# Optimization experiments

Measured on AMD Instinct MI355X. Metric: run time of the kernel, lower is better.

Reference implementation:

```python
import jax, jax.numpy as jnp
import numpy as np

B, S, H = 2, 2048, 4096
NH, HD = 32, 128          # heads, head_dim = H // NH
ROPE_THETA = 10000.0
CLIP_QKV = 8.0
SCALE = HD ** -0.5


def setup_inputs() -> dict:
    key = jax.random.key(0)
    k1, k2, k3 = jax.random.split(key, 3)
    hidden_states = jax.random.normal(k1, (B, S, H), dtype=jnp.float32)
    positions = jnp.arange(S, dtype=jnp.int32)
    # 0.02 init scale keeps qkv magnitudes realistic so the +/-8 clamp rarely saturates
    w_qkv = jax.random.normal(k2, (3 * H, H), dtype=jnp.float32) * 0.02
    w_o = jax.random.normal(k3, (H, H), dtype=jnp.float32) * 0.02
    return {"hidden_states": hidden_states, "positions": positions,
            "w_qkv": w_qkv, "w_o": w_o}


def _rope(x, positions):
    # x: [B, S, NH, HD]; neox-style rotary over full head_dim
    half = HD // 2
    inv_freq = 1.0 / (ROPE_THETA ** (jnp.arange(0, half, dtype=jnp.float32) / half))
    ang = positions.astype(jnp.float32)[:, None] * inv_freq[None, :]  # [S, half]
    cos = jnp.cos(ang)[None, :, None, :]
    sin = jnp.sin(ang)[None, :, None, :]
    x1, x2 = x[..., :half], x[..., half:]
    return jnp.concatenate([x1 * cos - x2 * sin, x2 * cos + x1 * sin], axis=-1)


def reference(hidden_states, positions, w_qkv, w_o):
    # fused QKV projection (no bias) + clamp
    qkv = jnp.einsum('bsh,oh->bso', hidden_states, w_qkv)
    qkv = jnp.clip(qkv, -CLIP_QKV, CLIP_QKV)
    q, k, v = jnp.split(qkv, 3, axis=-1)            # each [B, S, H]
    q = q.reshape(B, S, NH, HD)
    k = k.reshape(B, S, NH, HD)
    v = v.reshape(B, S, NH, HD)
    q = _rope(q, positions)
    k = _rope(k, positions)
    # causal attention
    scores = jnp.einsum('bqhd,bkhd->bhqk', q, k) * SCALE
    causal = jnp.tril(jnp.ones((S, S), dtype=bool))
    scores = jnp.where(causal[None, None], scores, jnp.finfo(scores.dtype).min)
    probs = jax.nn.softmax(scores, axis=-1)
    attn = jnp.einsum('bhqk,bkhd->bqhd', probs, v).reshape(B, S, H)
    return jnp.einsum('bsh,oh->bso', attn, w_o)
```

## Files before the change

### kernel.cpp

```cpp
#include <hip/hip_runtime.h>
#include <hip/hip_bf16.h>

#define BATCH 2
#define SEQ 2048
#define HID 4096
#define NHEAD 32
#define HDIM 128
#define BH (BATCH*NHEAD)
#define MROWS (BATCH*SEQ)
#define ATT_SCALE 0.08838834764831845f

typedef __attribute__((ext_vector_type(8))) short bf16x8;
typedef __attribute__((ext_vector_type(4))) float f32x4;

__device__ __forceinline__ float bf2f(short x){
  union { float f; unsigned u; } v; v.u = ((unsigned)(unsigned short)x) << 16; return v.f;
}
__device__ __forceinline__ short f2bf(float f){
  union { float f; unsigned u; } v; v.f = f;
  unsigned r = v.u + 0x7fffu + ((v.u >> 16) & 1u);
  return (short)(r >> 16);
}
__device__ __forceinline__ void gload_lds16(const void* g, void* l){
  __builtin_amdgcn_global_load_lds(
    (const __attribute__((address_space(1))) void*)g,
    (__attribute__((address_space(3))) void*)l, 16, 0, 0);
}

__global__ void cvt3_bf16(const float* __restrict__ a, short* __restrict__ ao, int na4,
                          const float* __restrict__ b, short* __restrict__ bo, int nb4,
                          const float* __restrict__ cc, short* __restrict__ co, int nc4){
  int i = blockIdx.x*blockDim.x + threadIdx.x;
  int stride = gridDim.x*blockDim.x;
  int tot = na4 + nb4 + nc4;
  for (; i < tot; i += stride){
    const float* src; short* dst; int k = i;
    if (k < na4){ src=a; dst=ao; }
    else if (k < na4+nb4){ k -= na4; src=b; dst=bo; }
    else { k -= na4+nb4; src=cc; dst=co; }
    float4 v = ((const float4*)src)[k];
    short4 o;
    o.x = f2bf(v.x); o.y = f2bf(v.y); o.z = f2bf(v.z); o.w = f2bf(v.w);
    ((short4*)dst)[k] = o;
  }
}

__global__ void rope_table_k(const int* __restrict__ pos, float* __restrict__ tab){
  int idx = blockIdx.x*blockDim.x + threadIdx.x;
  if (idx >= SEQ*64) return;
  int s = idx >> 6, d = idx & 63;
  float p = (float)pos[s];
  float inv = exp2f(-(float)d * (13.287712379549449f/64.0f));
  float ang = p * inv;
  tab[2*idx]   = cosf(ang);
  tab[2*idx+1] = sinf(ang);
}

template<int W>
__device__ __forceinline__ void stage_half(const short* __restrict__ gsrc, int ldg,
                                           short* lds, int tid, int h){
  #pragma unroll
  for (int li=0; li<2; ++li){
    int e16 = li*512 + tid;
    int rs = e16 >> 3, ck = e16 & 7;
    int r = ((rs/W)*2 + h)*W + (rs%W);
    gload_lds16(gsrc + (size_t)r*ldg + ((ck ^ (r&7))<<3),
                lds + r*64 + ck*8);
  }
}

__device__ __forceinline__ void read_ahalf(const short* Asb, int wr, int c, int g,
                                           int Mh, bf16x8 (&afr)[4][2]){
  #pragma unroll
  for (int mi=0; mi<4; ++mi){
    int row = wr*128 + (Mh*4+mi)*16 + c;
    const char* bp = (const char*)Asb + row*128;
    #pragma unroll
    for (int kk=0; kk<2; ++kk)
      afr[mi][kk] = *(const bf16x8*)(bp + ((kk*64 + g*16) ^ ((row&7)<<4)));
  }
}
__device__ __forceinline__ void read_bhalf(const short* Bsb, int wc, int c, int g,
                                           int Nh, bf16x8 (&bfr)[2][2]){
  #pragma unroll
  for (int ni=0; ni<2; ++ni){
    int row = wc*64 + (Nh*2+ni)*16 + c;
    const char* bp = (const char*)Bsb + row*128;
    #pragma unroll
    for (int kk=0; kk<2; ++kk)
      bfr[ni][kk] = *(const bf16x8*)(bp + ((kk*64 + g*16) ^ ((row&7)<<4)));
  }
}
template<int MH, int NHH>
__device__ __forceinline__ void mma_q(bf16x8 (&afr)[4][2], bf16x8 (&bfr)[2][2],
                                      f32x4 (&acc)[8][4]){
  #pragma unroll
  for (int kk=0; kk<2; ++kk)
    #pragma unroll
    for (int mi=0; mi<4; ++mi)
      #pragma unroll
      for (int ni=0; ni<2; ++ni)
        acc[MH*4+mi][NHH*2+ni] = __builtin_amdgcn_mfma_f32_16x16x32_bf16(
            afr[mi][kk], bfr[ni][kk], acc[MH*4+mi][NHH*2+ni], 0,0,0);
}

#define BAR()  asm volatile("s_barrier" ::: "memory")
#define LGK0() asm volatile("s_waitcnt lgkmcnt(0)" ::: "memory")
#define VMC6() asm volatile("s_waitcnt vmcnt(6)" ::: "memory")
#define VMC8() asm volatile("s_waitcnt vmcnt(8)" ::: "memory")
#define VMC0() asm volatile("s_waitcnt vmcnt(0)" ::: "memory")
#define SP1()  __builtin_amdgcn_s_setprio(1)
#define SP0()  __builtin_amdgcn_s_setprio(0)

template<int MODE>
__global__ __launch_bounds__(512, 2) void gemm8r(
    const short* __restrict__ A, const short* __restrict__ Bw,
    short* __restrict__ Qb, short* __restrict__ Kb, short* __restrict__ Vb,
    float* __restrict__ Of){
  __shared__ __align__(16) short As[2][256*64];
  __shared__ __align__(16) short Bs[2][256*64];
  const int K = HID;
  int tid = threadIdx.x, lane = tid & 63, w = tid >> 6;
  int wr = w >> 2, wc = w & 3, g = lane >> 4, c = lane & 15;
  int gx = gridDim.x;
  int nwg = gx * gridDim.y;
  int bid = blockIdx.y*gx + blockIdx.x;
  int cpx = nwg >> 3;
  int swz = (bid & 7)*cpx + (bid >> 3);
  int m0 = (swz / gx) * 256, n0 = (swz % gx) * 256;

  const short* Abase = A  + (size_t)m0*K;
  const short* Bbase = Bw + (size_t)n0*K;
  auto stageA = [&](int buf, int kt, int h){
    stage_half<64>(Abase + kt*64, K, &As[buf][0], tid, h);
  };
  auto stageB = [&](int buf, int kt, int h){
    stage_half<32>(Bbase + kt*64, K, &Bs[buf][0], tid, h);
  };

  f32x4 acc[8][4];
  f32x4 zero = {0.f,0.f,0.f,0.f};
  #pragma unroll
  for (int i=0;i<8;++i)
    #pragma unroll
    for (int j=0;j<4;++j) acc[i][j] = zero;
  bf16x8 afr[4][2], bfr0[2][2], bfr1[2][2];

  stageB(0,0,0); stageB(0,0,1); stageA(0,0,0); stageA(0,0,1);
  stageB(1,1,0); stageB(1,1,1); stageA(1,1,0); stageA(1,1,1);
  VMC8();
  BAR();

  const int NITER = K/128;
  for (int i = 0; i < NITER-1; ++i){
    int t2 = 2*i+2, t3 = 2*i+3;
    read_ahalf(&As[0][0], wr,c,g, 0, afr);
    read_bhalf(&Bs[0][0], wc,c,g, 0, bfr0);
    BAR(); LGK0(); SP1(); mma_q<0,0>(afr,bfr0,acc); SP0(); BAR();
    read_bhalf(&Bs[0][0], wc,c,g, 1, bfr1);
    stageB(0, t2, 0);
    BAR(); LGK0(); SP1(); mma_q<0,1>(afr,bfr1,acc); SP0(); BAR();
    read_ahalf(&As[0][0], wr,c,g, 1, afr);
    stageB(0, t2, 1); stageA(0, t2, 0);
    BAR(); LGK0(); SP1(); mma_q<1,1>(afr,bfr1,acc); SP0(); BAR();
    BAR(); LGK0(); SP1(); mma_q<1,0>(afr,bfr0,acc); SP0(); VMC6(); BAR();
    read_ahalf(&As[1][0], wr,c,g, 0, afr);
    read_bhalf(&Bs[1][0], wc,c,g, 0, bfr0);
    stageA(0, t2, 1);
    BAR(); LGK0(); SP1(); mma_q<0,0>(afr,bfr0,acc); SP0(); BAR();
    read_bhalf(&Bs[1][0], wc,c,g, 1, bfr1);
    stageB(1, t3, 0);
    BAR(); LGK0(); SP1(); mma_q<0,1>(afr,bfr1,acc); SP0(); BAR();
    read_ahalf(&As[1][0], wr,c,g, 1, afr);
    stageB(1, t3, 1); stageA(1, t3, 0);
    BAR(); LGK0(); SP1(); mma_q<1,1>(afr,bfr1,acc); SP0(); BAR();
    stageA(1, t3, 1);
    BAR(); LGK0(); SP1(); mma_q<1,0>(afr,bfr0,acc); SP0(); VMC8(); BAR();
  }
  {
    read_ahalf(&As[0][0], wr,c,g, 0, afr);
    read_bhalf(&Bs[0][0], wc,c,g, 0, bfr0);
    BAR(); LGK0(); SP1(); mma_q<0,0>(afr,bfr0,acc); SP0(); BAR();
    read_bhalf(&Bs[0][0], wc,c,g, 1, bfr1);
    BAR(); LGK0(); SP1(); mma_q<0,1>(afr,bfr1,acc); SP0(); BAR();
    read_ahalf(&As[0][0], wr,c,g, 1, afr);
    BAR(); LGK0(); SP1(); mma_q<1,1>(afr,bfr1,acc); SP0(); BAR();
    BAR(); LGK0(); SP1(); mma_q<1,0>(afr,bfr0,acc); SP0(); VMC0(); BAR();
    read_ahalf(&As[1][0], wr,c,g, 0, afr);
    read_bhalf(&Bs[1][0], wc,c,g, 0, bfr0);
    BAR(); LGK0(); SP1(); mma_q<0,0>(afr,bfr0,acc); SP0(); BAR();
    read_bhalf(&Bs[1][0], wc,c,g, 1, bfr1);
    BAR(); LGK0(); SP1(); mma_q<0,1>(afr,bfr1,acc); SP0(); BAR();
    read_ahalf(&As[1][0], wr,c,g, 1, afr);
    BAR(); LGK0(); SP1(); mma_q<1,1>(afr,bfr1,acc); SP0(); BAR();
    BAR(); LGK0(); SP1(); mma_q<1,0>(afr,bfr0,acc); SP0(); BAR();
  }

  #pragma unroll
  for (int fa=0; fa<8; ++fa){
    #pragma unroll
    for (int fb=0; fb<4; ++fb){
      f32x4 v = acc[fa][fb];
      #pragma unroll
      for (int rr=0; rr<4; ++rr){
        int row = m0 + wr*128 + fa*16 + g*4 + rr;
        int col = n0 + wc*64  + fb*16 + c;
        float x = v[rr];
        if (MODE == 0){
          x = fminf(fmaxf(x, -8.0f), 8.0f);
          int sel = col >> 12, wi = col & 4095;
          int head = wi >> 7, d = wi & 127;
          int b = row >> 11, s = row & 2047;
          size_t off = ((size_t)(b*NHEAD + head)*SEQ + s)*HDIM + d;
          short* dst = (sel == 0) ? Qb : (sel == 1) ? Kb : Vb;
          dst[off] = f2bf(x);
        } else {
          Of[(size_t)row*HID + col] = x;
        }
      }
    }
  }
}

__global__ void rope_apply_k(short* __restrict__ Qb, short* __restrict__ Kb,
                             const float* __restrict__ tab){
  int idx = blockIdx.x*blockDim.x + threadIdx.x;
  if (idx >= BH*SEQ*8) return;
  int t = idx & 7;
  int s = (idx >> 3) & (SEQ-1);
  int bh = idx >> 14;
  size_t base = ((size_t)bh*SEQ + s)*HDIM + t*8;
  const float* tb = tab + 2*(s*64 + t*8);
  bf16x8 q1 = *(bf16x8*)(Qb+base), q2 = *(bf16x8*)(Qb+base+64);
  bf16x8 k1 = *(bf16x8*)(Kb+base), k2 = *(bf16x8*)(Kb+base+64);
  bf16x8 o1, o2, p1, p2;
  #pragma unroll
  for (int u=0;u<8;++u){
    float cs = tb[2*u], sn = tb[2*u+1];
    float a = bf2f(q1[u]), b = bf2f(q2[u]);
    o1[u] = f2bf(a*cs - b*sn); o2[u] = f2bf(b*cs + a*sn);
    a = bf2f(k1[u]); b = bf2f(k2[u]);
    p1[u] = f2bf(a*cs - b*sn); p2[u] = f2bf(b*cs + a*sn);
  }
  *(bf16x8*)(Qb+base)    = o1; *(bf16x8*)(Qb+base+64) = o2;
  *(bf16x8*)(Kb+base)    = p1; *(bf16x8*)(Kb+base+64) = p2;
}

__global__ void transpose_v_k(const short* __restrict__ V, short* __restrict__ Vt){
  __shared__ short t[32][33];
  int bh = blockIdx.z;
  int s0 = blockIdx.x*32, d0 = blockIdx.y*32;
  int tx = threadIdx.x & 31, ty = threadIdx.x >> 5;
  const short* src = V + ((size_t)bh*SEQ + s0)*HDIM + d0;
  #pragma unroll
  for (int i=ty;i<32;i+=8) t[i][tx] = src[(size_t)i*HDIM + tx];
  __syncthreads();
  short* dst = Vt + ((size_t)bh*HDIM + d0)*SEQ + s0;
  #pragma unroll
  for (int i=ty;i<32;i+=8) dst[(size_t)i*SEQ + tx] = t[tx][i];
}

__global__ __launch_bounds__(256) void flash_attn_k(
    const short* __restrict__ Qb, const short* __restrict__ Kb,
    const short* __restrict__ Vt, short* __restrict__ attn){
  __shared__ short Ks[2][64*128];
  __shared__ short Vs[2][128*64];
  __shared__ short Ps[4][16][72];
  int tid = threadIdx.x, lane = tid & 63, w = tid >> 6;
  int g = lane >> 4, c = lane & 15;
  int flat = blockIdx.y*gridDim.x + blockIdx.x;
  int xcd = flat & 7, idx = flat >> 3;
  int bh = xcd + 8*(idx >> 5);
  int qblk = 31 - (idx & 31);
  int q0 = qblk * 64;
  int qw = q0 + w*16;
  bf16x8 qf[4];
  #pragma unroll
  for (int ks=0;ks<4;++ks)
    qf[ks] = *(const bf16x8*)(Qb + ((size_t)bh*SEQ + qw + c)*HDIM + ks*32 + g*8);
  f32x4 o[8];
  f32x4 zero = {0.f,0.f,0.f,0.f};
  #pragma unroll
  for (int i=0;i<8;++i) o[i] = zero;
  float m_r[4] = {-1e30f,-1e30f,-1e30f,-1e30f};
  float l_r[4] = {0.f,0.f,0.f,0.f};

  auto stage = [&](int j, int b){
    int kv0 = j*64;
    #pragma unroll
    for (int i=0;i<4;++i){
      int e = i*256 + tid;
      int kr = e >> 4, kc = e & 15;
      gload_lds16(Kb + ((size_t)bh*SEQ + kv0 + kr)*HDIM + (size_t)((kc ^ (kr&7))*8),
                  &Ks[b][kr*128 + kc*8]);
      int vr = e >> 3, vc = e & 7;
      gload_lds16(Vt + ((size_t)bh*HDIM + vr)*SEQ + kv0 + (size_t)((vc ^ (vr&7))*8),
                  &Vs[b][vr*64 + vc*8]);
    }
  };

  stage(0, 0);
  __syncthreads();
  int buf = 0;
  for (int j=0;j<=qblk;++j){
    if (j < qblk) stage(j+1, buf^1);

    int kv0 = j*64;
    f32x4 sf[4];
    #pragma unroll
    for (int fj=0;fj<4;++fj) sf[fj] = zero;
    __builtin_amdgcn_s_setprio(1);
    #pragma unroll
    for (int ks=0;ks<4;++ks){
      #pragma unroll
      for (int fj=0;fj<4;++fj){
        int kvrow = fj*16 + c;
        bf16x8 kb = *(const bf16x8*)&Ks[buf][kvrow*128 + (((ks*4+g) ^ (c&7))*8)];
        sf[fj] = __builtin_amdgcn_mfma_f32_16x16x32_bf16(qf[ks], kb, sf[fj], 0,0,0);
      }
    }
    __builtin_amdgcn_s_setprio(0);
    bool diag = (j == qblk);
    float rmax[4];
    #pragma unroll
    for (int rr=0;rr<4;++rr){
      #pragma unroll
      for (int fj=0;fj<4;++fj){
        float v = sf[fj][rr] * ATT_SCALE;
        if (diag && (kv0 + fj*16 + c) > (qw + g*4 + rr)) v = -1e30f;
        sf[fj][rr] = v;
      }
      float t = fmaxf(fmaxf(sf[0][rr], sf[1][rr]), fmaxf(sf[2][rr], sf[3][rr]));
      t = fmaxf(t, __shfl_xor(t, 1));
      t = fmaxf(t, __shfl_xor(t, 2));
      t = fmaxf(t, __shfl_xor(t, 4));
      t = fmaxf(t, __shfl_xor(t, 8));
      rmax[rr] = t;
    }
    float alpha[4];
    #pragma unroll
    for (int rr=0;rr<4;++rr){
      float mnew = fmaxf(m_r[rr], rmax[rr]);
      alpha[rr] = __expf(m_r[rr] - mnew);
      m_r[rr] = mnew;
      float ps = 0.f;
      #pragma unroll
      for (int fj=0;fj<4;++fj){
        float p = __expf(sf[fj][rr] - mnew);
        sf[fj][rr] = p;
        ps += p;
      }
      ps += __shfl_xor(ps, 1);
      ps += __shfl_xor(ps, 2);
      ps += __shfl_xor(ps, 4);
      ps += __shfl_xor(ps, 8);
      l_r[rr] = l_r[rr]*alpha[rr] + ps;
    }
    #pragma unroll
    for (int ni=0;ni<8;++ni){
      f32x4 t = o[ni];
      t[0]*=alpha[0]; t[1]*=alpha[1]; t[2]*=alpha[2]; t[3]*=alpha[3];
      o[ni] = t;
    }
    #pragma unroll
    for (int fj=0;fj<4;++fj)
      #pragma unroll
      for (int rr=0;rr<4;++rr)
        Ps[w][g*4+rr][fj*16+c] = f2bf(sf[fj][rr]);
    __builtin_amdgcn_s_setprio(1);
    #pragma unroll
    for (int ks=0;ks<2;++ks){
      bf16x8 pa = *(const bf16x8*)&Ps[w][c][ks*32 + g*8];
      #pragma unroll
      for (int ni=0;ni<8;++ni){
        int d = ni*16 + c;
        bf16x8 vb = *(const bf16x8*)&Vs[buf][d*64 + (((ks*4+g) ^ (c&7))*8)];
        o[ni] = __builtin_amdgcn_mfma_f32_16x16x32_bf16(pa, vb, o[ni], 0,0,0);
      }
    }
    __builtin_amdgcn_s_setprio(0);
    __syncthreads();
    buf ^= 1;
  }
  int b = bh >> 5, h = bh & 31;
  #pragma unroll
  for (int rr=0;rr<4;++rr){
    float inv = 1.0f / l_r[rr];
    int s = qw + g*4 + rr;
    #pragma unroll
    for (int ni=0;ni<8;++ni){
      int d = ni*16 + c;
      attn[((size_t)(b*SEQ + s))*HID + h*HDIM + d] = f2bf(o[ni][rr] * inv);
    }
  }
}

extern "C" void kernel_launch(void* const* d_in, const int* in_sizes, int n_in,
                              void* d_out, int out_size, void* d_ws, size_t ws_size,
                              hipStream_t stream){
  const float* hs   = (const float*)d_in[0];
  const int*   pos  = (const int*)d_in[1];
  const float* wqkv = (const float*)d_in[2];
  const float* wo   = (const float*)d_in[3];
  float* out = (float*)d_out;
  char* ws = (char*)d_ws;
  size_t off = 0;
  auto alloc = [&](size_t bytes){ void* p = ws + off; off += (bytes + 255) & ~(size_t)255; return p; };
  short* hsb   = (short*)alloc((size_t)MROWS*HID*2);
  short* wqkvb = (short*)alloc((size_t)3*HID*HID*2);
  short* wob   = (short*)alloc((size_t)HID*HID*2);
  short* Qb    = (short*)alloc((size_t)BH*SEQ*HDIM*2);
  short* Kb    = (short*)alloc((size_t)BH*SEQ*HDIM*2);
  short* Vb    = (short*)alloc((size_t)BH*SEQ*HDIM*2);
  short* Vt    = (short*)alloc((size_t)BH*SEQ*HDIM*2);
  short* attn  = (short*)alloc((size_t)MROWS*HID*2);
  float* tab   = (float*)alloc((size_t)SEQ*64*2*4);
  (void)ws_size; (void)in_sizes; (void)n_in; (void)out_size;

  cvt3_bf16<<<2048,256,0,stream>>>(hs, hsb, MROWS*HID/4,
                                   wqkv, wqkvb, 3*HID*HID/4,
                                   wo, wob, HID*HID/4);
  rope_table_k<<<(SEQ*64+255)/256,256,0,stream>>>(pos, tab);
  gemm8r<0><<<dim3(48,16),512,0,stream>>>(hsb, wqkvb, Qb, Kb, Vb, nullptr);
  rope_apply_k<<<(BH*SEQ*8+255)/256,256,0,stream>>>(Qb, Kb, tab);
  transpose_v_k<<<dim3(SEQ/32, HDIM/32, BH),256,0,stream>>>(Vb, Vt);
  flash_attn_k<<<dim3(SEQ/64, BH),256,0,stream>>>(Qb, Kb, Vt, attn);
  gemm8r<1><<<dim3(16,16),512,0,stream>>>(attn, wob, nullptr, nullptr, nullptr, out);
}
```

Baseline: 819.0 us.

## Prefetch B fragments across GEMM phases; fold scale into Q; lazy softmax rescale

The GEMM main loop now issues the B-fragment LDS reads one phase earlier, during the previous MFMA block, so they overlap with compute instead of stalling before it. The vmcnt waits are moved to match. Attention folds softmax_scale*log2(e) into Q during RoPE and switches to exp2f, removing a multiply per score element. The running max and output rescale now happen only when some row's max grows by more than 8, which skips most alpha multiplies. The trade-offs are bf16 rounding of the scaled Q and possible loss of precision if unnormalised exponents grow large; the new pipeline ordering also risks LDS read/write races.

```diff
diff --git a/kernel.cpp b/kernel.cpp
--- a/kernel.cpp
+++ b/kernel.cpp
@@ -8,7 +8,7 @@
 #define HDIM 128
 #define BH (BATCH*NHEAD)
 #define MROWS (BATCH*SEQ)
-#define ATT_SCALE 0.08838834764831845f
+#define SC2 0.1275187963f
 
 typedef __attribute__((ext_vector_type(8))) short bf16x8;
 typedef __attribute__((ext_vector_type(4))) float f32x4;
@@ -113,7 +113,7 @@
 #define SP0()  __builtin_amdgcn_s_setprio(0)
 
 template<int MODE>
-__global__ __launch_bounds__(512, 2) void gemm8r(
+__global__ __launch_bounds__(512, 2) void gemm8s(
     const short* __restrict__ A, const short* __restrict__ Bw,
     short* __restrict__ Qb, short* __restrict__ Kb, short* __restrict__ Vb,
     float* __restrict__ Of){
@@ -150,46 +150,49 @@
   stageB(1,1,0); stageB(1,1,1); stageA(1,1,0); stageA(1,1,1);
   VMC8();
   BAR();
+  read_bhalf(&Bs[0][0], wc,c,g, 0, bfr0);
+  read_bhalf(&Bs[0][0], wc,c,g, 1, bfr1);
 
   const int NITER = K/128;
   for (int i = 0; i < NITER-1; ++i){
     int t2 = 2*i+2, t3 = 2*i+3;
     read_ahalf(&As[0][0], wr,c,g, 0, afr);
-    read_bhalf(&Bs[0][0], wc,c,g, 0, bfr0);
     BAR(); LGK0(); SP1(); mma_q<0,0>(afr,bfr0,acc); SP0(); BAR();
-    read_bhalf(&Bs[0][0], wc,c,g, 1, bfr1);
     stageB(0, t2, 0);
     BAR(); LGK0(); SP1(); mma_q<0,1>(afr,bfr1,acc); SP0(); BAR();
     read_ahalf(&As[0][0], wr,c,g, 1, afr);
     stageB(0, t2, 1); stageA(0, t2, 0);
-    BAR(); LGK0(); SP1(); mma_q<1,1>(afr,bfr1,acc); SP0(); BAR();
-    BAR(); LGK0(); SP1(); mma_q<1,0>(afr,bfr0,acc); SP0(); VMC6(); BAR();
+    BAR(); LGK0(); SP1(); mma_q<1,1>(afr,bfr1,acc); SP0(); VMC6(); BAR();
+    read_bhalf(&Bs[1][0], wc,c,g, 1, bfr1);
+    BAR(); LGK0(); SP1(); mma_q<1,0>(afr,bfr0,acc); SP0();
+    read_bhalf(&Bs[1][0], wc,c,g, 0, bfr0);
+    BAR();
     read_ahalf(&As[1][0], wr,c,g, 0, afr);
-    read_bhalf(&Bs[1][0], wc,c,g, 0, bfr0);
     stageA(0, t2, 1);
     BAR(); LGK0(); SP1(); mma_q<0,0>(afr,bfr0,acc); SP0(); BAR();
-    read_bhalf(&Bs[1][0], wc,c,g, 1, bfr1);
     stageB(1, t3, 0);
     BAR(); LGK0(); SP1(); mma_q<0,1>(afr,bfr1,acc); SP0(); BAR();
     read_ahalf(&As[1][0], wr,c,g, 1, afr);
     stageB(1, t3, 1); stageA(1, t3, 0);
-    BAR(); LGK0(); SP1(); mma_q<1,1>(afr,bfr1,acc); SP0(); BAR();
+    BAR(); LGK0(); SP1(); mma_q<1,1>(afr,bfr1,acc); SP0(); VMC6(); BAR();
     stageA(1, t3, 1);
-    BAR(); LGK0(); SP1(); mma_q<1,0>(afr,bfr0,acc); SP0(); VMC8(); BAR();
+    read_bhalf(&Bs[0][0], wc,c,g, 1, bfr1);
+    BAR(); LGK0(); SP1(); mma_q<1,0>(afr,bfr0,acc); SP0();
+    read_bhalf(&Bs[0][0], wc,c,g, 0, bfr0);
+    BAR();
   }
   {
     read_ahalf(&As[0][0], wr,c,g, 0, afr);
-    read_bhalf(&Bs[0][0], wc,c,g, 0, bfr0);
     BAR(); LGK0(); SP1(); mma_q<0,0>(afr,bfr0,acc); SP0(); BAR();
-    read_bhalf(&Bs[0][0], wc,c,g, 1, bfr1);
     BAR(); LGK0(); SP1(); mma_q<0,1>(afr,bfr1,acc); SP0(); BAR();
     read_ahalf(&As[0][0], wr,c,g, 1, afr);
-    BAR(); LGK0(); SP1(); mma_q<1,1>(afr,bfr1,acc); SP0(); BAR();
-    BAR(); LGK0(); SP1(); mma_q<1,0>(afr,bfr0,acc); SP0(); VMC0(); BAR();
+    BAR(); LGK0(); SP1(); mma_q<1,1>(afr,bfr1,acc); SP0(); VMC0(); BAR();
+    read_bhalf(&Bs[1][0], wc,c,g, 1, bfr1);
+    BAR(); LGK0(); SP1(); mma_q<1,0>(afr,bfr0,acc); SP0();
+    read_bhalf(&Bs[1][0], wc,c,g, 0, bfr0);
+    BAR();
     read_ahalf(&As[1][0], wr,c,g, 0, afr);
-    read_bhalf(&Bs[1][0], wc,c,g, 0, bfr0);
     BAR(); LGK0(); SP1(); mma_q<0,0>(afr,bfr0,acc); SP0(); BAR();
-    read_bhalf(&Bs[1][0], wc,c,g, 1, bfr1);
     BAR(); LGK0(); SP1(); mma_q<0,1>(afr,bfr1,acc); SP0(); BAR();
     read_ahalf(&As[1][0], wr,c,g, 1, afr);
     BAR(); LGK0(); SP1(); mma_q<1,1>(afr,bfr1,acc); SP0(); BAR();
@@ -238,7 +241,7 @@
   for (int u=0;u<8;++u){
     float cs = tb[2*u], sn = tb[2*u+1];
     float a = bf2f(q1[u]), b = bf2f(q2[u]);
-    o1[u] = f2bf(a*cs - b*sn); o2[u] = f2bf(b*cs + a*sn);
+    o1[u] = f2bf((a*cs - b*sn)*SC2); o2[u] = f2bf((b*cs + a*sn)*SC2);
     a = bf2f(k1[u]); b = bf2f(k2[u]);
     p1[u] = f2bf(a*cs - b*sn); p2[u] = f2bf(b*cs + a*sn);
   }
@@ -324,11 +327,10 @@
     float rmax[4];
     #pragma unroll
     for (int rr=0;rr<4;++rr){
-      #pragma unroll
-      for (int fj=0;fj<4;++fj){
-        float v = sf[fj][rr] * ATT_SCALE;
-        if (diag && (kv0 + fj*16 + c) > (qw + g*4 + rr)) v = -1e30f;
-        sf[fj][rr] = v;
+      if (diag){
+        #pragma unroll
+        for (int fj=0;fj<4;++fj)
+          if ((kv0 + fj*16 + c) > (qw + g*4 + rr)) sf[fj][rr] = -1e30f;
       }
       float t = fmaxf(fmaxf(sf[0][rr], sf[1][rr]), fmaxf(sf[2][rr], sf[3][rr]));
       t = fmaxf(t, __shfl_xor(t, 1));
@@ -337,16 +339,30 @@
       t = fmaxf(t, __shfl_xor(t, 8));
       rmax[rr] = t;
     }
-    float alpha[4];
+    bool need = (rmax[0] > m_r[0] + 8.0f) | (rmax[1] > m_r[1] + 8.0f) |
+                (rmax[2] > m_r[2] + 8.0f) | (rmax[3] > m_r[3] + 8.0f);
+    if (__any(need)){
+      float alpha[4];
+      #pragma unroll
+      for (int rr=0;rr<4;++rr){
+        float mnew = fmaxf(m_r[rr], rmax[rr]);
+        alpha[rr] = exp2f(m_r[rr] - mnew);
+        m_r[rr] = mnew;
+        l_r[rr] *= alpha[rr];
+      }
+      #pragma unroll
+      for (int ni=0;ni<8;++ni){
+        f32x4 t = o[ni];
+        t[0]*=alpha[0]; t[1]*=alpha[1]; t[2]*=alpha[2]; t[3]*=alpha[3];
+        o[ni] = t;
+      }
+    }
     #pragma unroll
     for (int rr=0;rr<4;++rr){
-      float mnew = fmaxf(m_r[rr], rmax[rr]);
-      alpha[rr] = __expf(m_r[rr] - mnew);
-      m_r[rr] = mnew;
       float ps = 0.f;
       #pragma unroll
       for (int fj=0;fj<4;++fj){
-        float p = __expf(sf[fj][rr] - mnew);
+        float p = exp2f(sf[fj][rr] - m_r[rr]);
         sf[fj][rr] = p;
         ps += p;
       }
@@ -354,13 +370,7 @@
       ps += __shfl_xor(ps, 2);
       ps += __shfl_xor(ps, 4);
       ps += __shfl_xor(ps, 8);
-      l_r[rr] = l_r[rr]*alpha[rr] + ps;
-    }
-    #pragma unroll
-    for (int ni=0;ni<8;++ni){
-      f32x4 t = o[ni];
-      t[0]*=alpha[0]; t[1]*=alpha[1]; t[2]*=alpha[2]; t[3]*=alpha[3];
-      o[ni] = t;
+      l_r[rr] += ps;
     }
     #pragma unroll
     for (int fj=0;fj<4;++fj)
@@ -421,9 +431,9 @@
                                    wqkv, wqkvb, 3*HID*HID/4,
                                    wo, wob, HID*HID/4);
   rope_table_k<<<(SEQ*64+255)/256,256,0,stream>>>(pos, tab);
-  gemm8r<0><<<dim3(48,16),512,0,stream>>>(hsb, wqkvb, Qb, Kb, Vb, nullptr);
+  gemm8s<0><<<dim3(48,16),512,0,stream>>>(hsb, wqkvb, Qb, Kb, Vb, nullptr);
   rope_apply_k<<<(BH*SEQ*8+255)/256,256,0,stream>>>(Qb, Kb, tab);
   transpose_v_k<<<dim3(SEQ/32, HDIM/32, BH),256,0,stream>>>(Vb, Vt);
   flash_attn_k<<<dim3(SEQ/64, BH),256,0,stream>>>(Qb, Kb, Vt, attn);
-  gemm8r<1><<<dim3(16,16),512,0,stream>>>(attn, wob, nullptr, nullptr, nullptr, out);
-}
+  gemm8s<1><<<dim3(16,16),512,0,stream>>>(attn, wob, nullptr, nullptr, nullptr, out);
+}
```

Result: slower. 849.6 us (+3.7%).
